# Kernel tuning notes

Hardware: AMD Instinct MI355X
Metric: run time of the kernel (lower is better)

Reference implementation:

```python
import jax, jax.numpy as jnp
import numpy as np

NSITES = 100000
NYEARS = 20
NVIS = 2
HDIM = 64


def setup_inputs() -> dict:
    key = jax.random.key(0)
    ks = jax.random.split(key, 10)
    def w(k, shape, fan_in):
        return (jax.random.normal(k, shape, jnp.float32) / np.sqrt(fan_in)).astype(jnp.float32)
    return {
        "sxy0": jax.random.normal(ks[0], (1, NSITES, 1), jnp.float32),
        "sxy": jax.random.normal(ks[1], (NSITES, NYEARS - 1, 1), jnp.float32),
        "oxy": jax.random.normal(ks[2], (NSITES, NYEARS, NVIS), jnp.float32),
        # to_h0: Linear(1 -> 64)
        "W_h0": w(ks[3], (HDIM, 1), 1), "b_h0": jnp.zeros((HDIM,), jnp.float32),
        # to_h1: Linear(64 -> 64)
        "W_h1": w(ks[4], (HDIM, HDIM), HDIM), "b_h1": jnp.zeros((HDIM,), jnp.float32),
        # to_hrnn: RNN(input=1, hidden=64, relu)
        "W_ih": w(ks[5], (HDIM, 1), 1), "b_ih": jnp.zeros((HDIM,), jnp.float32),
        "W_hh": w(ks[6], (HDIM, HDIM), HDIM), "b_hh": jnp.zeros((HDIM,), jnp.float32),
        # to_psi0 / to_psi: Linear(64 -> 1)
        "W_psi0": w(ks[7], (1, HDIM), HDIM), "b_psi0": jnp.zeros((1,), jnp.float32),
        "W_psi": w(ks[8], (1, HDIM), HDIM), "b_psi": jnp.zeros((1,), jnp.float32),
        # to_p: Linear(65 -> 1)
        "W_p": w(ks[9], (1, HDIM + 1), HDIM + 1), "b_p": jnp.zeros((1,), jnp.float32),
    }


def reference(sxy0, sxy, oxy, W_h0, b_h0, W_h1, b_h1, W_ih, b_ih, W_hh, b_hh,
              W_psi0, b_psi0, W_psi, b_psi, W_p, b_p):
    # site embeddings -> initial hidden state
    hs = jax.nn.elu(sxy0 @ W_h0.T + b_h0)            # [1, N, H]
    h0 = jax.nn.elu(hs @ W_h1.T + b_h1)              # [1, N, H]

    # single-layer relu RNN, batch_first: sxy [N, T, 1], h0 [1, N, H]
    xs = jnp.swapaxes(sxy, 0, 1)                     # [T, N, 1]
    def step(h, x):
        h_new = jax.nn.relu(x @ W_ih.T + b_ih + h @ W_hh.T + b_hh)
        return h_new, h_new
    _, h_seq = jax.lax.scan(step, h0[0], xs)         # [T, N, H]
    h_out = jnp.swapaxes(h_seq, 0, 1)                # [N, T, H]

    psi0_out = jax.nn.sigmoid(h0 @ W_psi0.T + b_psi0)   # [1, N, 1]
    psi_out = jax.nn.sigmoid(h_out @ W_psi.T + b_psi)   # [N, T, 1]

    # detection prob p[i, t, j] = sigmoid(to_p(cat(H[i, t], oxy[i, t, j])))
    # where H[:, 0] = h0 and H[:, t] = h_out[:, t-1] for t >= 1
    H = jnp.concatenate([h0[0][:, None, :], h_out], axis=1)  # [N, Y, H]
    logits = H @ W_p[:, :HDIM].T + oxy * W_p[0, HDIM] + b_p  # [N, Y, NVIS]
    p = jax.nn.sigmoid(logits)
    return psi0_out, psi_out, p
```

## Files before the change

kernel.cpp:

```cpp
#include <hip/hip_runtime.h>
#include <math.h>

#define NSITES 100000
#define NYEARS 20
#define HDIM 64
#define WSTR 72

typedef __bf16 bf16x8 __attribute__((ext_vector_type(8)));
typedef float f32x4 __attribute__((ext_vector_type(4)));

__device__ __forceinline__ float sigmoidf_(float x) { return 1.0f / (1.0f + __expf(-x)); }
__device__ __forceinline__ float eluf_(float x) { return x > 0.0f ? x : expm1f(x); }

__device__ __forceinline__ unsigned pack2_(float a, float b) {
    union { __bf16 h; unsigned short u; } x, y;
    x.h = (__bf16)a; y.h = (__bf16)b;
    return ((unsigned)y.u << 16) | (unsigned)x.u;
}

__device__ __forceinline__ bf16x8 cvt8_(const float* p) {
    float4 a = ((const float4*)p)[0];
    float4 b = ((const float4*)p)[1];
    bf16x8 r;
    r[0] = (__bf16)a.x; r[1] = (__bf16)a.y; r[2] = (__bf16)a.z; r[3] = (__bf16)a.w;
    r[4] = (__bf16)b.x; r[5] = (__bf16)b.y; r[6] = (__bf16)b.z; r[7] = (__bf16)b.w;
    return r;
}

__device__ __forceinline__ bf16x8 ldsfrag_(const unsigned short* b, int row, int off) {
    union { bf16x8 v; uint4 u; } r;
    r.u = *(const uint4*)&b[row * WSTR + off];
    return r.v;
}

__device__ __forceinline__ bf16x8 pack_bf_(f32x4 lo, f32x4 hi) {
    bf16x8 r;
    r[0] = (__bf16)lo[0]; r[1] = (__bf16)lo[1]; r[2] = (__bf16)lo[2]; r[3] = (__bf16)lo[3];
    r[4] = (__bf16)hi[0]; r[5] = (__bf16)hi[1]; r[6] = (__bf16)hi[2]; r[7] = (__bf16)hi[3];
    return r;
}

__global__ __launch_bounds__(128)
void rnet_kernel(const float* __restrict__ sxy0,
                 const float* __restrict__ sxy,
                 const float* __restrict__ oxy,
                 const float* __restrict__ W_h0, const float* __restrict__ b_h0,
                 const float* __restrict__ W_h1, const float* __restrict__ b_h1,
                 const float* __restrict__ W_ih, const float* __restrict__ b_ih,
                 const float* __restrict__ W_hh, const float* __restrict__ b_hh,
                 const float* __restrict__ W_psi0, const float* __restrict__ b_psi0,
                 const float* __restrict__ W_psi, const float* __restrict__ b_psi,
                 const float* __restrict__ W_p, const float* __restrict__ b_p,
                 float* __restrict__ out)
{
    const int tid  = threadIdx.x;
    const int lane = tid & 63;
    const int wv   = tid >> 6;
    const int s = lane & 15;
    const int q = lane >> 4;
    const int sq = s >> 2, sr = s & 3;
    const int base = blockIdx.x * 32;
    const int sl   = wv * 16 + s;
    const int site = base + sl;

    __shared__ __align__(16) unsigned short whh_l[64 * WSTR];
    __shared__ __align__(16) unsigned short wh1_l[64 * WSTR];
    __shared__ __align__(16) float xs_sh[32 * 19];

    float* pL    = (float*)wh1_l;
    float* psiL  = pL + 640;
    float* psi0L = psiL + 640;

    float* __restrict__ out_psi0 = out;
    float* __restrict__ out_psi  = out + NSITES;
    float* __restrict__ out_p    = out + 20 * NSITES;

    {
        const float4* whg = (const float4*)W_hh;
        const float4* w1g = (const float4*)W_h1;
#pragma unroll
        for (int j = 0; j < 8; ++j) {
            int e4 = j * 128 + tid;
            int row = e4 >> 4, c4 = e4 & 15;
            float4 a = whg[e4];
            uint2 pa; pa.x = pack2_(a.x, a.y); pa.y = pack2_(a.z, a.w);
            *(uint2*)&whh_l[row * WSTR + c4 * 4] = pa;
            float4 b = w1g[e4];
            uint2 pb; pb.x = pack2_(b.x, b.y); pb.y = pack2_(b.z, b.w);
            *(uint2*)&wh1_l[row * WSTR + c4 * 4] = pb;
        }
        const float* src = sxy + (size_t)base * (NYEARS - 1);
#pragma unroll
        for (int r = 0; r < 5; ++r) {
            int i = r * 128 + tid;
            if (i < 32 * (NYEARS - 1)) xs_sh[i] = src[i];
        }
    }
    __syncthreads();

    bf16x8 bf[2];
    {
        const float s0v = sxy0[site];
        bf16x8 bf0[2];
#pragma unroll
        for (int kt = 0; kt < 2; ++kt) {
            const float* wp = W_h0 + kt * 32 + q * 8;
            const float* bp = b_h0 + kt * 32 + q * 8;
            float4 w0 = ((const float4*)wp)[0], w1 = ((const float4*)wp)[1];
            float4 c0 = ((const float4*)bp)[0], c1 = ((const float4*)bp)[1];
            float v[8];
            v[0] = eluf_(fmaf(s0v, w0.x, c0.x)); v[1] = eluf_(fmaf(s0v, w0.y, c0.y));
            v[2] = eluf_(fmaf(s0v, w0.z, c0.z)); v[3] = eluf_(fmaf(s0v, w0.w, c0.w));
            v[4] = eluf_(fmaf(s0v, w1.x, c1.x)); v[5] = eluf_(fmaf(s0v, w1.y, c1.y));
            v[6] = eluf_(fmaf(s0v, w1.z, c1.z)); v[7] = eluf_(fmaf(s0v, w1.w, c1.w));
#pragma unroll
            for (int j = 0; j < 8; ++j) bf0[kt][j] = (__bf16)v[j];
        }

        f32x4 acc[4];
#pragma unroll
        for (int mt = 0; mt < 4; ++mt) {
            const int dr = 32 * (mt >> 1) + 8 * q + 4 * (mt & 1);
            float4 b1 = *(const float4*)(b_h1 + dr);
            acc[mt][0] = b1.x; acc[mt][1] = b1.y; acc[mt][2] = b1.z; acc[mt][3] = b1.w;
        }
#pragma unroll
        for (int kt = 0; kt < 2; ++kt)
#pragma unroll
            for (int mt = 0; mt < 4; ++mt) {
                const int ar = 32 * (mt >> 1) + 8 * sq + 4 * (mt & 1) + sr;
                bf16x8 a = ldsfrag_(wh1_l, ar, kt * 32 + q * 8);
                acc[mt] = __builtin_amdgcn_mfma_f32_16x16x32_bf16(a, bf0[kt], acc[mt], 0, 0, 0);
            }
        f32x4 e[4];
#pragma unroll
        for (int mt = 0; mt < 4; ++mt)
#pragma unroll
            for (int r = 0; r < 4; ++r) e[mt][r] = eluf_(acc[mt][r]);
        bf[0] = pack_bf_(e[0], e[1]);
        bf[1] = pack_bf_(e[2], e[3]);
    }

    bf16x8 a_hh[4][2];
#pragma unroll
    for (int mt = 0; mt < 4; ++mt) {
        const int ar = 32 * (mt >> 1) + 8 * sq + 4 * (mt & 1) + sr;
#pragma unroll
        for (int kt = 0; kt < 2; ++kt)
            a_hh[mt][kt] = ldsfrag_(whh_l, ar, kt * 32 + q * 8);
    }
    bf16x8 a_head[2];
    {
        const float* hrow = (s == 1) ? W_p : ((s == 2) ? W_psi0 : W_psi);
#pragma unroll
        for (int kt = 0; kt < 2; ++kt) a_head[kt] = cvt8_(hrow + kt * 32 + q * 8);
    }
    f32x4 biasD[4], wihD[4];
#pragma unroll
    for (int mt = 0; mt < 4; ++mt) {
        const int dr = 32 * (mt >> 1) + 8 * q + 4 * (mt & 1);
        float4 bi = *(const float4*)(b_ih + dr);
        float4 bh = *(const float4*)(b_hh + dr);
        float4 wi = *(const float4*)(W_ih + dr);
        biasD[mt][0] = bi.x + bh.x; biasD[mt][1] = bi.y + bh.y;
        biasD[mt][2] = bi.z + bh.z; biasD[mt][3] = bi.w + bh.w;
        wihD[mt][0] = wi.x; wihD[mt][1] = wi.y; wihD[mt][2] = wi.z; wihD[mt][3] = wi.w;
    }
    f32x4 headC;
    headC[0] = (q == 0) ? b_psi[0]  : 0.0f;
    headC[1] = (q == 0) ? b_p[0]    : 0.0f;
    headC[2] = (q == 0) ? b_psi0[0] : 0.0f;
    headC[3] = 0.0f;

    __syncthreads();

#pragma unroll 1
    for (int t = 1; t < NYEARS; ++t) {
        const float x = xs_sh[sl * 19 + (t - 1)];

        f32x4 acc[4], accH;
#pragma unroll
        for (int mt = 0; mt < 4; ++mt)
            acc[mt] = __builtin_amdgcn_mfma_f32_16x16x32_bf16(a_hh[mt][0], bf[0], biasD[mt], 0, 0, 0);
        accH = __builtin_amdgcn_mfma_f32_16x16x32_bf16(a_head[0], bf[0], headC, 0, 0, 0);
#pragma unroll
        for (int mt = 0; mt < 4; ++mt)
            acc[mt] = __builtin_amdgcn_mfma_f32_16x16x32_bf16(a_hh[mt][1], bf[1], acc[mt], 0, 0, 0);
        accH = __builtin_amdgcn_mfma_f32_16x16x32_bf16(a_head[1], bf[1], accH, 0, 0, 0);

        f32x4 hn[4];
#pragma unroll
        for (int mt = 0; mt < 4; ++mt)
#pragma unroll
            for (int r = 0; r < 4; ++r)
                hn[mt][r] = fmaxf(fmaf(x, wihD[mt][r], acc[mt][r]), 0.0f);
        bf[0] = pack_bf_(hn[0], hn[1]);
        bf[1] = pack_bf_(hn[2], hn[3]);

        if (q == 0) {
            pL[sl * 20 + (t - 1)]   = accH[1];
            psiL[sl * 20 + (t - 1)] = accH[0];
            if (t == 1) psi0L[sl] = accH[2];
        }
    }

    {
        f32x4 accH = __builtin_amdgcn_mfma_f32_16x16x32_bf16(a_head[0], bf[0], headC, 0, 0, 0);
        accH = __builtin_amdgcn_mfma_f32_16x16x32_bf16(a_head[1], bf[1], accH, 0, 0, 0);
        if (q == 0) {
            pL[sl * 20 + 19]   = accH[1];
            psiL[sl * 20 + 19] = accH[0];
        }
    }

    __syncthreads();

    const float wpo = W_p[HDIM];
    if (tid < 32) out_psi0[base + tid] = sigmoidf_(psi0L[tid]);
#pragma unroll
    for (int r = 0; r < 5; ++r) {
        int i = r * 128 + tid;
        if (i < 32 * 19) {
            int s2 = i / 19, c = i - s2 * 19;
            out_psi[(size_t)base * 19 + i] = sigmoidf_(psiL[s2 * 20 + c + 1]);
        }
    }
    const float4* oxy_b = (const float4*)(oxy + (size_t)base * 40);
    float4* outp_b = (float4*)(out_p + (size_t)base * 40);
#pragma unroll
    for (int r = 0; r < 3; ++r) {
        int i4 = r * 128 + tid;
        if (i4 < 320) {
            float4 ox = oxy_b[i4];
            float lg0 = pL[i4 * 2];
            float lg1 = pL[i4 * 2 + 1];
            float4 pv;
            pv.x = sigmoidf_(fmaf(wpo, ox.x, lg0));
            pv.y = sigmoidf_(fmaf(wpo, ox.y, lg0));
            pv.z = sigmoidf_(fmaf(wpo, ox.z, lg1));
            pv.w = sigmoidf_(fmaf(wpo, ox.w, lg1));
            outp_b[i4] = pv;
        }
    }
}

extern "C" void kernel_launch(void* const* d_in, const int* in_sizes, int n_in,
                              void* d_out, int out_size, void* d_ws, size_t ws_size,
                              hipStream_t stream) {
    const float* sxy0   = (const float*)d_in[0];
    const float* sxy    = (const float*)d_in[1];
    const float* oxy    = (const float*)d_in[2];
    const float* W_h0   = (const float*)d_in[3];
    const float* b_h0   = (const float*)d_in[4];
    const float* W_h1   = (const float*)d_in[5];
    const float* b_h1   = (const float*)d_in[6];
    const float* W_ih   = (const float*)d_in[7];
    const float* b_ih   = (const float*)d_in[8];
    const float* W_hh   = (const float*)d_in[9];
    const float* b_hh   = (const float*)d_in[10];
    const float* W_psi0 = (const float*)d_in[11];
    const float* b_psi0 = (const float*)d_in[12];
    const float* W_psi  = (const float*)d_in[13];
    const float* b_psi  = (const float*)d_in[14];
    const float* W_p    = (const float*)d_in[15];
    const float* b_p    = (const float*)d_in[16];

    float* out = (float*)d_out;

    dim3 block(128);
    dim3 grid(NSITES / 32);
    rnet_kernel<<<grid, block, 0, stream>>>(
        sxy0, sxy, oxy, W_h0, b_h0, W_h1, b_h1, W_ih, b_ih, W_hh, b_hh,
        W_psi0, b_psi0, W_psi, b_psi, W_p, b_p, out);
}
```

Baseline: 144.9 us.

## Process 64 sites per 256-thread block and prefetch RNN inputs

Doubles the block to 256 threads covering 64 sites, so the bf16 weight staging into LDS is amortized over twice as many sites, and adds bounds clamping because 100000 is not a multiple of 64. Head outputs now go to dedicated LDS buffers instead of aliasing the W_h1 buffer, which removes a barrier before the recurrence. The next timestep's input is loaded one iteration ahead. In exchange the block uses more LDS and the grid has half as many blocks, which may lower occupancy or load balance.

After: 138.1 us. 4.7% less time.

```diff
diff --git a/kernel.cpp b/kernel.cpp
--- a/kernel.cpp
+++ b/kernel.cpp
@@ -40,7 +40,7 @@
     return r;
 }
 
-__global__ __launch_bounds__(128)
+__global__ __launch_bounds__(256, 2)
 void rnet_kernel(const float* __restrict__ sxy0,
                  const float* __restrict__ sxy,
                  const float* __restrict__ oxy,
@@ -59,17 +59,17 @@
     const int s = lane & 15;
     const int q = lane >> 4;
     const int sq = s >> 2, sr = s & 3;
-    const int base = blockIdx.x * 32;
+    const int base = blockIdx.x * 64;
     const int sl   = wv * 16 + s;
     const int site = base + sl;
+    const int site_ld = site < NSITES ? site : NSITES - 1;
 
     __shared__ __align__(16) unsigned short whh_l[64 * WSTR];
     __shared__ __align__(16) unsigned short wh1_l[64 * WSTR];
-    __shared__ __align__(16) float xs_sh[32 * 19];
-
-    float* pL    = (float*)wh1_l;
-    float* psiL  = pL + 640;
-    float* psi0L = psiL + 640;
+    __shared__ __align__(16) float xs_sh[64 * 19];
+    __shared__ __align__(16) float pL[64 * 20];
+    __shared__ __align__(16) float psiL[64 * 20];
+    __shared__ __align__(16) float psi0L[64];
 
     float* __restrict__ out_psi0 = out;
     float* __restrict__ out_psi  = out + NSITES;
@@ -79,8 +79,8 @@
         const float4* whg = (const float4*)W_hh;
         const float4* w1g = (const float4*)W_h1;
 #pragma unroll
-        for (int j = 0; j < 8; ++j) {
-            int e4 = j * 128 + tid;
+        for (int j = 0; j < 4; ++j) {
+            int e4 = j * 256 + tid;
             int row = e4 >> 4, c4 = e4 & 15;
             float4 a = whg[e4];
             uint2 pa; pa.x = pack2_(a.x, a.y); pa.y = pack2_(a.z, a.w);
@@ -89,18 +89,21 @@
             uint2 pb; pb.x = pack2_(b.x, b.y); pb.y = pack2_(b.z, b.w);
             *(uint2*)&wh1_l[row * WSTR + c4 * 4] = pb;
         }
-        const float* src = sxy + (size_t)base * (NYEARS - 1);
 #pragma unroll
         for (int r = 0; r < 5; ++r) {
-            int i = r * 128 + tid;
-            if (i < 32 * (NYEARS - 1)) xs_sh[i] = src[i];
+            int i = r * 256 + tid;
+            if (i < 64 * 19) {
+                int srow = i / 19, c = i - srow * 19;
+                int gsite = base + srow; if (gsite >= NSITES) gsite = NSITES - 1;
+                xs_sh[i] = sxy[(size_t)gsite * 19 + c];
+            }
         }
     }
     __syncthreads();
 
     bf16x8 bf[2];
     {
-        const float s0v = sxy0[site];
+        const float s0v = sxy0[site_ld];
         bf16x8 bf0[2];
 #pragma unroll
         for (int kt = 0; kt < 2; ++kt) {
@@ -172,11 +175,10 @@
     headC[2] = (q == 0) ? b_psi0[0] : 0.0f;
     headC[3] = 0.0f;
 
-    __syncthreads();
-
+    float x = xs_sh[sl * 19];
 #pragma unroll 1
     for (int t = 1; t < NYEARS; ++t) {
-        const float x = xs_sh[sl * 19 + (t - 1)];
+        float x_next = (t < NYEARS - 1) ? xs_sh[sl * 19 + t] : 0.0f;
 
         f32x4 acc[4], accH;
 #pragma unroll
@@ -202,6 +204,7 @@
             psiL[sl * 20 + (t - 1)] = accH[0];
             if (t == 1) psi0L[sl] = accH[2];
         }
+        x = x_next;
     }
 
     {
@@ -216,21 +219,22 @@
     __syncthreads();
 
     const float wpo = W_p[HDIM];
-    if (tid < 32) out_psi0[base + tid] = sigmoidf_(psi0L[tid]);
+    if (tid < 64 && base + tid < NSITES) out_psi0[base + tid] = sigmoidf_(psi0L[tid]);
 #pragma unroll
     for (int r = 0; r < 5; ++r) {
-        int i = r * 128 + tid;
-        if (i < 32 * 19) {
+        int i = r * 256 + tid;
+        if (i < 64 * 19 && (size_t)base * 19 + i < (size_t)NSITES * 19) {
             int s2 = i / 19, c = i - s2 * 19;
             out_psi[(size_t)base * 19 + i] = sigmoidf_(psiL[s2 * 20 + c + 1]);
         }
     }
     const float4* oxy_b = (const float4*)(oxy + (size_t)base * 40);
     float4* outp_b = (float4*)(out_p + (size_t)base * 40);
+    const int p4max = (NSITES * 40) / 4;
 #pragma unroll
     for (int r = 0; r < 3; ++r) {
-        int i4 = r * 128 + tid;
-        if (i4 < 320) {
+        int i4 = r * 256 + tid;
+        if (i4 < 640 && blockIdx.x * 640 + i4 < p4max) {
             float4 ox = oxy_b[i4];
             float lg0 = pL[i4 * 2];
             float lg1 = pL[i4 * 2 + 1];
@@ -267,8 +271,8 @@
 
     float* out = (float*)d_out;
 
-    dim3 block(128);
-    dim3 grid(NSITES / 32);
+    dim3 block(256);
+    dim3 grid((NSITES + 63) / 64);
     rnet_kernel<<<grid, block, 0, stream>>>(
         sxy0, sxy, oxy, W_h0, b_h0, W_h1, b_h1, W_ih, b_ih, W_hh, b_hh,
         W_psi0, b_psi0, W_psi, b_psi, W_p, b_p, out);
```
